# Kernel tuning notes

Hardware: AMD Instinct MI355X
Metric: run time of the kernel (lower is better)

## Reference

```python
import jax, jax.numpy as jnp
import numpy as np

N, F = 12288, 512
NEG_INF = jnp.float32(-1e9)  # matches Keras BaseDenseAttention mask additive constant


def setup_inputs() -> dict:
    key = jax.random.key(0)
    k1, k2 = jax.random.split(key)
    features = jax.random.normal(k1, (N, F), dtype=jnp.float32)
    A = jax.random.randint(k2, (N, N), 0, 2).astype(jnp.int32)
    return {"features": features, "A": A}


def reference(features, A):
    # Keras Attention with query=key=value=dropout(features); dropout is identity
    # at inference. use_scale=False -> plain dot-product scores, no 1/sqrt(d).
    scores = jnp.einsum("nf,mf->nm", features, features)          # [N, N]
    scores = jnp.where(A > 0, scores, NEG_INF)                    # mask non-edges
    attn = jax.nn.softmax(scores, axis=-1)                        # softmax over keys
    return jnp.einsum("nm,mf->nf", attn, features)                # [N, F]
```

## Files before the change

### kernel.cpp

```cpp
#include <hip/hip_runtime.h>
#include <cstddef>
#include <cstdint>

#define NN 12288
#define FF 512
#define NWORDS (NN / 32)
#define NKT (NN / 128)
#define CMP_BLOCKS ((NN * NWORDS) / 256)
#define PREP_BLOCKS ((NN / 32) * (FF / 32))

using half8 = __attribute__((ext_vector_type(8))) _Float16;
using half4 = __attribute__((ext_vector_type(4))) _Float16;
using f32x4 = __attribute__((ext_vector_type(4))) float;

constexpr float MASK_NEG = -1e9f;

__device__ __forceinline__ void gll16(const void* g, void* l) {
    __builtin_amdgcn_global_load_lds((const __attribute__((address_space(1))) void*)g,
                                     (__attribute__((address_space(3))) void*)l, 16, 0, 0);
}

#define PHASE(N)                                                        \
    do {                                                                \
        asm volatile("s_waitcnt vmcnt(" #N ")" ::: "memory");           \
        __builtin_amdgcn_s_barrier();                                   \
        __builtin_amdgcn_sched_barrier(0);                              \
    } while (0)

__global__ __launch_bounds__(256)
void prepass_fused(const int* __restrict__ Amat, uint32_t* __restrict__ Abits,
                   const float* __restrict__ in, _Float16* __restrict__ feath,
                   _Float16* __restrict__ featT) {
    const int bid = blockIdx.x;
    if (bid < CMP_BLOCKS) {
        const size_t W = (size_t)bid * 256 + threadIdx.x;
        const int4* p = reinterpret_cast<const int4*>(Amat + W * 32);
        uint32_t b = 0;
#pragma unroll
        for (int q = 0; q < 8; ++q) {
            const int4 v = p[q];
            b |= (uint32_t)(v.x > 0) << (4 * q + 0);
            b |= (uint32_t)(v.y > 0) << (4 * q + 1);
            b |= (uint32_t)(v.z > 0) << (4 * q + 2);
            b |= (uint32_t)(v.w > 0) << (4 * q + 3);
        }
        Abits[W] = b;
    } else {
        __shared__ float tile[32][33];
        const int b2 = bid - CMP_BLOCKS;
        const int bi = b2 % (NN / 32);
        const int bj = b2 / (NN / 32);
        const int r  = threadIdx.x >> 3;
        const int c4 = (threadIdx.x & 7) << 2;
        float4 v = *reinterpret_cast<const float4*>(in + (size_t)(bi * 32 + r) * FF + bj * 32 + c4);
        tile[r][c4 + 0] = v.x; tile[r][c4 + 1] = v.y; tile[r][c4 + 2] = v.z; tile[r][c4 + 3] = v.w;
        half4 hr;
        hr[0] = (_Float16)v.x; hr[1] = (_Float16)v.y; hr[2] = (_Float16)v.z; hr[3] = (_Float16)v.w;
        *reinterpret_cast<half4*>(feath + (size_t)(bi * 32 + r) * FF + bj * 32 + c4) = hr;
        __syncthreads();
        half4 h;
#pragma unroll
        for (int k = 0; k < 4; ++k) h[k] = (_Float16)tile[c4 + k][r];
        *reinterpret_cast<half4*>(featT + (size_t)(bj * 32 + r) * NN + bi * 32 + c4) = h;
    }
}

__global__ void cvt_feat_kernel(const float* __restrict__ in, _Float16* __restrict__ out) {
    const size_t i = ((size_t)blockIdx.x * blockDim.x + threadIdx.x) * 8;
    float4 x = *reinterpret_cast<const float4*>(in + i);
    float4 y = *reinterpret_cast<const float4*>(in + i + 4);
    half8 h;
    h[0] = (_Float16)x.x; h[1] = (_Float16)x.y; h[2] = (_Float16)x.z; h[3] = (_Float16)x.w;
    h[4] = (_Float16)y.x; h[5] = (_Float16)y.y; h[6] = (_Float16)y.z; h[7] = (_Float16)y.w;
    *reinterpret_cast<half8*>(out + i) = h;
}

__global__ __launch_bounds__(256)
void gemm1_exp(const _Float16* __restrict__ feath, const uint32_t* __restrict__ Abits,
               _Float16* __restrict__ Pmat, float* __restrict__ m_t, _Float16* __restrict__ s_t) {
    __shared__ alignas(16) _Float16 As[3][128 * 32];
    __shared__ alignas(16) _Float16 Bs[3][128 * 32];
    __shared__ alignas(16) float rowmax2[128][2];
    __shared__ alignas(16) float rowsum2[128][2];

    const int tid = threadIdx.x, lane = tid & 63, wid = tid >> 6;
    const int g = lane >> 4, a = lane & 15;
    const int wr = wid >> 1, wc = wid & 1;
    const int row0 = blockIdx.x * 128, col0 = blockIdx.y * 128;

    f32x4 acc[4][4];
#pragma unroll
    for (int i = 0; i < 4; ++i)
#pragma unroll
        for (int j = 0; j < 4; ++j) acc[i][j] = f32x4{0.f, 0.f, 0.f, 0.f};

    const int lr  = lane >> 2;
    const int sl  = lane & 3;
    const int lsw = (sl ^ ((lr >> 1) & 3)) * 8;
    const int rk  = (a >> 1) & 3;

    auto stage = [&](int buf, int t) {
#pragma unroll
        for (int c = 0; c < 2; ++c) {
            const int ch = wid * 2 + c;
            gll16(feath + (size_t)(row0 + ch * 16 + lr) * FF + t * 32 + lsw, &As[buf][ch * 512]);
            gll16(feath + (size_t)(col0 + ch * 16 + lr) * FF + t * 32 + lsw, &Bs[buf][ch * 512]);
        }
    };

    stage(0, 0);
    stage(1, 1);
#pragma unroll
    for (int t = 0; t < 16; ++t) {
        if (t < 15) PHASE(4);
        else        PHASE(0);
        const int cb = t % 3;
        half8 af[4], bf[4];
#pragma unroll
        for (int rf = 0; rf < 4; ++rf)
            af[rf] = *reinterpret_cast<const half8*>(&As[cb][(64 * wr + 16 * rf + a) * 32 + ((g ^ rk) << 3)]);
#pragma unroll
        for (int cf = 0; cf < 4; ++cf)
            bf[cf] = *reinterpret_cast<const half8*>(&Bs[cb][(64 * wc + 16 * cf + a) * 32 + ((g ^ rk) << 3)]);
#pragma unroll
        for (int rf = 0; rf < 4; ++rf)
#pragma unroll
            for (int cf = 0; cf < 4; ++cf)
                acc[rf][cf] = __builtin_amdgcn_mfma_f32_16x16x32_f16(af[rf], bf[cf], acc[rf][cf], 0, 0, 0);
        if (t + 2 < 16) stage((t + 2) % 3, t + 2);
    }

    const int cw0 = (col0 + 64 * wc) >> 5;
    uint2 am[4][4];
#pragma unroll
    for (int rf = 0; rf < 4; ++rf)
#pragma unroll
        for (int r = 0; r < 4; ++r) {
            const int grow = row0 + 64 * wr + 16 * rf + 4 * g + r;
            am[rf][r] = *reinterpret_cast<const uint2*>(&Abits[(size_t)grow * NWORDS + cw0]);
        }
#pragma unroll
    for (int rf = 0; rf < 4; ++rf)
#pragma unroll
        for (int r = 0; r < 4; ++r)
#pragma unroll
            for (int cf = 0; cf < 4; ++cf) {
                const uint32_t w = (cf < 2) ? am[rf][r].x : am[rf][r].y;
                const uint32_t bit = (w >> (a + 16 * (cf & 1))) & 1u;
                acc[rf][cf][r] = bit ? acc[rf][cf][r] : MASK_NEG;
            }

#pragma unroll
    for (int rf = 0; rf < 4; ++rf)
#pragma unroll
        for (int r = 0; r < 4; ++r) {
            float v = fmaxf(fmaxf(acc[rf][0][r], acc[rf][1][r]), fmaxf(acc[rf][2][r], acc[rf][3][r]));
            v = fmaxf(v, __shfl_xor(v, 1, 16));
            v = fmaxf(v, __shfl_xor(v, 2, 16));
            v = fmaxf(v, __shfl_xor(v, 4, 16));
            v = fmaxf(v, __shfl_xor(v, 8, 16));
            if (a == 0) rowmax2[64 * wr + 16 * rf + 4 * g + r][wc] = v;
        }
    __syncthreads();

#pragma unroll
    for (int rf = 0; rf < 4; ++rf)
#pragma unroll
        for (int r = 0; r < 4; ++r) {
            const int lrow = 64 * wr + 16 * rf + 4 * g + r;
            const float mt = fmaxf(rowmax2[lrow][0], rowmax2[lrow][1]);
            const size_t rbase = (size_t)(row0 + lrow) * NN + col0 + 64 * wc + a;
            float ps = 0.f;
#pragma unroll
            for (int cf = 0; cf < 4; ++cf) {
                const float p = __expf(acc[rf][cf][r] - mt);
                ps += p;
                Pmat[rbase + 16 * cf] = (_Float16)p;
            }
            ps += __shfl_xor(ps, 1, 16);
            ps += __shfl_xor(ps, 2, 16);
            ps += __shfl_xor(ps, 4, 16);
            ps += __shfl_xor(ps, 8, 16);
            if (a == 0) rowsum2[lrow][wc] = ps;
        }
    __syncthreads();
    if (tid < 128) {
        m_t[(size_t)blockIdx.y * NN + row0 + tid] = fmaxf(rowmax2[tid][0], rowmax2[tid][1]);
        s_t[(size_t)blockIdx.y * NN + row0 + tid] = (_Float16)(rowsum2[tid][0] + rowsum2[tid][1]);
    }
}

__global__ __launch_bounds__(256)
void stats_kernel(const float* __restrict__ m_t, const _Float16* __restrict__ s_t,
                  _Float16* __restrict__ sc_t, float* __restrict__ l_row) {
    const int r = blockIdx.x * 256 + threadIdx.x;
    float m = -3.0e38f;
#pragma unroll 4
    for (int kt = 0; kt < NKT; ++kt) m = fmaxf(m, m_t[(size_t)kt * NN + r]);
    float l = 0.f;
#pragma unroll 4
    for (int kt = 0; kt < NKT; ++kt) {
        const float e = __expf(m_t[(size_t)kt * NN + r] - m);
        sc_t[(size_t)kt * NN + r] = (_Float16)e;
        l += e * (float)s_t[(size_t)kt * NN + r];
    }
    l_row[r] = l;
}

__global__ __launch_bounds__(256)
void gemm2_scale(const _Float16* __restrict__ Pmat, const _Float16* __restrict__ featT,
                 const _Float16* __restrict__ sc_t, const float* __restrict__ l_row,
                 float* __restrict__ out) {
    __shared__ alignas(16) _Float16 As[2][128 * 64];
    __shared__ alignas(16) _Float16 Bs[2][64 * 64];

    const int tid = threadIdx.x, lane = tid & 63, wid = tid >> 6;
    const int g = lane >> 4, a = lane & 15;
    const int wr = wid >> 1, wc = wid & 1;
    const int row0 = blockIdx.x * 128, col0 = blockIdx.y * 64;

    f32x4 acc[4][2];
#pragma unroll
    for (int i = 0; i < 4; ++i) { acc[i][0] = f32x4{0.f,0.f,0.f,0.f}; acc[i][1] = f32x4{0.f,0.f,0.f,0.f}; }

    const int l8  = lane >> 3;
    const int sc8 = lane & 7;
    const int xk  = a & 7;
    const size_t scbase = row0 + 64 * wr + a;

    auto stage = [&](int buf, int t) {
#pragma unroll
        for (int c = 0; c < 4; ++c) {
            const int seg = wid * 4 + c;
            const int row = seg * 8 + l8;
            gll16(Pmat + (size_t)(row0 + row) * NN + t * 64 + ((sc8 ^ l8) << 3),
                  &As[buf][seg * 512]);
        }
#pragma unroll
        for (int c = 0; c < 2; ++c) {
            const int seg = wid * 2 + c;
            const int row = seg * 8 + l8;
            gll16(featT + (size_t)(col0 + row) * NN + t * 64 + ((sc8 ^ l8) << 3),
                  &Bs[buf][seg * 512]);
        }
    };

    _Float16 pend[4], sc[4];
#pragma unroll
    for (int rf = 0; rf < 4; ++rf) pend[rf] = sc_t[scbase + 16 * rf];

    stage(0, 0);
    __syncthreads();
    int buf = 0;
    for (int t = 0; t < 192; ++t) {
        if ((t & 1) == 0) {
#pragma unroll
            for (int rf = 0; rf < 4; ++rf) sc[rf] = pend[rf];
            const int ktn = (t >> 1) + 1;
            if (ktn < NKT) {
#pragma unroll
                for (int rf = 0; rf < 4; ++rf)
                    pend[rf] = sc_t[(size_t)ktn * NN + scbase + 16 * rf];
            }
        }
        if (t + 1 < 192) stage(buf ^ 1, t + 1);
#pragma unroll
        for (int kk = 0; kk < 2; ++kk) {
            const int c8r = ((kk << 2) + g) ^ xk;
            half8 af[4], bf[2];
#pragma unroll
            for (int rf = 0; rf < 4; ++rf) {
                const int row = 64 * wr + 16 * rf + a;
                af[rf] = *reinterpret_cast<const half8*>(&As[buf][row * 64 + (c8r << 3)]);
                af[rf] = af[rf] * sc[rf];
            }
#pragma unroll
            for (int cf = 0; cf < 2; ++cf) {
                const int row = 32 * wc + 16 * cf + a;
                bf[cf] = *reinterpret_cast<const half8*>(&Bs[buf][row * 64 + (c8r << 3)]);
            }
#pragma unroll
            for (int rf = 0; rf < 4; ++rf)
#pragma unroll
                for (int cf = 0; cf < 2; ++cf)
                    acc[rf][cf] = __builtin_amdgcn_mfma_f32_16x16x32_f16(af[rf], bf[cf], acc[rf][cf], 0, 0, 0);
        }
        __syncthreads();
        buf ^= 1;
    }

#pragma unroll
    for (int rf = 0; rf < 4; ++rf)
#pragma unroll
        for (int r = 0; r < 4; ++r) {
            const int grow = row0 + 64 * wr + 16 * rf + 4 * g + r;
            const float il = 1.0f / l_row[grow];
#pragma unroll
            for (int cf = 0; cf < 2; ++cf) {
                const int gcol = col0 + 32 * wc + 16 * cf + a;
                out[(size_t)grow * FF + gcol] = acc[rf][cf][r] * il;
            }
        }
}

constexpr int BM_ = 64;
constexpr int BN_ = 64;
constexpr int KV_STRIDE = 520;

template<bool RH>
__global__ __launch_bounds__(512, 2)
void attn_flash(const float* __restrict__ featf, const _Float16* __restrict__ feath,
                const int* __restrict__ Amat, float* __restrict__ out) {
    __shared__ alignas(16) _Float16 kv[BN_ * KV_STRIDE];
    __shared__ alignas(16) _Float16 pbuf[BM_][72];
    __shared__ alignas(16) float pmax[BM_][2];
    __shared__ alignas(16) float psum[BM_][2];
    __shared__ alignas(16) float m_s[BM_];
    __shared__ alignas(16) float l_s[BM_];
    __shared__ alignas(16) float rscale[BM_];

    const int tid  = threadIdx.x;
    const int lane = tid & 63;
    const int wid  = tid >> 6;
    const int g    = lane >> 4;
    const int a    = lane & 15;
    const int rg   = wid >> 1;
    const int ch   = wid & 1;
    const int qrow0 = blockIdx.x * BM_;

    half8 qf[16];
    {
        const int qr = qrow0 + 16 * rg + a;
#pragma unroll
        for (int ks = 0; ks < 16; ++ks) {
            const int f0 = 32 * ks + 8 * g;
            if constexpr (RH) {
                qf[ks] = *reinterpret_cast<const half8*>(feath + (size_t)qr * FF + f0);
            } else {
                const float* sp = featf + (size_t)qr * FF + f0;
                float4 x = *reinterpret_cast<const float4*>(sp);
                float4 y = *reinterpret_cast<const float4*>(sp + 4);
                half8 h;
                h[0] = (_Float16)x.x; h[1] = (_Float16)x.y; h[2] = (_Float16)x.z; h[3] = (_Float16)x.w;
                h[4] = (_Float16)y.x; h[5] = (_Float16)y.y; h[6] = (_Float16)y.z; h[7] = (_Float16)y.w;
                qf[ks] = h;
            }
        }
    }

    f32x4 acc[4][4];
#pragma unroll
    for (int i = 0; i < 4; ++i)
#pragma unroll
        for (int j = 0; j < 4; ++j) acc[i][j] = f32x4{0.f, 0.f, 0.f, 0.f};

    if (tid < BM_) { m_s[tid] = -INFINITY; l_s[tid] = 0.f; }
    __syncthreads();

    for (int kt = 0; kt < NN / BN_; ++kt) {
        const int key0 = kt * BN_;
#pragma unroll
        for (int i = 0; i < 8; ++i) {
            const int flat8 = tid + i * 512;
            const int key   = flat8 >> 6;
            const int b     = flat8 & 63;
            const int slot  = (b + (key >> 3)) & 63;
            _Float16* dst = &kv[key * KV_STRIDE + slot * 8];
            if constexpr (RH) {
                *reinterpret_cast<half8*>(dst) =
                    *reinterpret_cast<const half8*>(feath + (size_t)(key0 + key) * FF + b * 8);
            } else {
                const float* sp = featf + (size_t)(key0 + key) * FF + b * 8;
                float4 x = *reinterpret_cast<const float4*>(sp);
                float4 y = *reinterpret_cast<const float4*>(sp + 4);
                half8 h;
                h[0] = (_Float16)x.x; h[1] = (_Float16)x.y; h[2] = (_Float16)x.z; h[3] = (_Float16)x.w;
                h[4] = (_Float16)y.x; h[5] = (_Float16)y.y; h[6] = (_Float16)y.z; h[7] = (_Float16)y.w;
                *reinterpret_cast<half8*>(dst) = h;
            }
        }

        int am[2][4];
#pragma unroll
        for (int fc = 0; fc < 2; ++fc)
#pragma unroll
            for (int r = 0; r < 4; ++r) {
                const int arow = qrow0 + 16 * rg + 4 * g + r;
                const int acol = key0 + 32 * ch + 16 * fc + a;
                am[fc][r] = Amat[(size_t)arow * NN + acol];
            }
        __syncthreads();

        f32x4 s0{0.f, 0.f, 0.f, 0.f}, s1{0.f, 0.f, 0.f, 0.f};
        const int bk0 = 32 * ch + a;
        const int bk1 = bk0 + 16;
        const int kb0 = bk0 >> 3;
        const int kb1 = bk1 >> 3;
        const _Float16* kr0 = &kv[bk0 * KV_STRIDE];
        const _Float16* kr1 = &kv[bk1 * KV_STRIDE];
#pragma unroll
        for (int ks = 0; ks < 16; ++ks) {
            const int b = 4 * ks + g;
            const half8 bf0 = *reinterpret_cast<const half8*>(kr0 + (((b + kb0) & 63) << 3));
            const half8 bf1 = *reinterpret_cast<const half8*>(kr1 + (((b + kb1) & 63) << 3));
            s0 = __builtin_amdgcn_mfma_f32_16x16x32_f16(qf[ks], bf0, s0, 0, 0, 0);
            s1 = __builtin_amdgcn_mfma_f32_16x16x32_f16(qf[ks], bf1, s1, 0, 0, 0);
        }

        float sv[2][4];
#pragma unroll
        for (int r = 0; r < 4; ++r) {
            sv[0][r] = (am[0][r] > 0) ? s0[r] : MASK_NEG;
            sv[1][r] = (am[1][r] > 0) ? s1[r] : MASK_NEG;
        }
#pragma unroll
        for (int r = 0; r < 4; ++r) {
            float v = fmaxf(sv[0][r], sv[1][r]);
            v = fmaxf(v, __shfl_xor(v, 1, 16));
            v = fmaxf(v, __shfl_xor(v, 2, 16));
            v = fmaxf(v, __shfl_xor(v, 4, 16));
            v = fmaxf(v, __shfl_xor(v, 8, 16));
            if (a == 0) pmax[16 * rg + 4 * g + r][ch] = v;
        }
        __syncthreads();

#pragma unroll
        for (int r = 0; r < 4; ++r) {
            const int row = 16 * rg + 4 * g + r;
            const float mo = m_s[row];
            const float mn = fmaxf(mo, fmaxf(pmax[row][0], pmax[row][1]));
            const float p0 = __expf(sv[0][r] - mn);
            const float p1 = __expf(sv[1][r] - mn);
            pbuf[row][32 * ch + a]      = (_Float16)p0;
            pbuf[row][32 * ch + 16 + a] = (_Float16)p1;
            float ssum = p0 + p1;
            ssum += __shfl_xor(ssum, 1, 16);
            ssum += __shfl_xor(ssum, 2, 16);
            ssum += __shfl_xor(ssum, 4, 16);
            ssum += __shfl_xor(ssum, 8, 16);
            if (a == 0) psum[row][ch] = ssum;
        }
        __syncthreads();

        if (tid < BM_) {
            const float mo = m_s[tid];
            const float mn = fmaxf(mo, fmaxf(pmax[tid][0], pmax[tid][1]));
            const float sc = __expf(mo - mn);
            l_s[tid] = l_s[tid] * sc + psum[tid][0] + psum[tid][1];
            m_s[tid] = mn;
            rscale[tid] = sc;
        }
        __syncthreads();

#pragma unroll
        for (int rf = 0; rf < 4; ++rf) {
            const float4 scv = *reinterpret_cast<const float4*>(&rscale[16 * rf + 4 * g]);
#pragma unroll
            for (int cf = 0; cf < 4; ++cf) {
                acc[rf][cf][0] *= scv.x; acc[rf][cf][1] *= scv.y;
                acc[rf][cf][2] *= scv.z; acc[rf][cf][3] *= scv.w;
            }
        }
#pragma unroll
        for (int kk = 0; kk < 2; ++kk) {
            half8 af[4];
#pragma unroll
            for (int rf = 0; rf < 4; ++rf)
                af[rf] = *reinterpret_cast<const half8*>(&pbuf[16 * rf + a][32 * kk + 8 * g]);
            const int keybase = 32 * kk + 8 * g;
#pragma unroll
            for (int cf = 0; cf < 4; ++cf) {
                const int col  = 64 * wid + 16 * cf + a;
                const int slot = (((col >> 3) + 4 * kk + g) & 63);
                const _Float16* vb = &kv[(size_t)keybase * KV_STRIDE + (slot << 3) + (col & 7)];
                half8 bf;
#pragma unroll
                for (int j = 0; j < 8; ++j)
                    bf[j] = vb[j * KV_STRIDE];
#pragma unroll
                for (int rf = 0; rf < 4; ++rf)
                    acc[rf][cf] = __builtin_amdgcn_mfma_f32_16x16x32_f16(af[rf], bf, acc[rf][cf], 0, 0, 0);
            }
        }
        __syncthreads();
    }

#pragma unroll
    for (int rf = 0; rf < 4; ++rf) {
        const float4 lv = *reinterpret_cast<const float4*>(&l_s[16 * rf + 4 * g]);
        const float inv[4] = {1.f / lv.x, 1.f / lv.y, 1.f / lv.z, 1.f / lv.w};
#pragma unroll
        for (int cf = 0; cf < 4; ++cf) {
            const int col = 64 * wid + 16 * cf + a;
#pragma unroll
            for (int r = 0; r < 4; ++r) {
                out[(size_t)(qrow0 + 16 * rf + 4 * g + r) * FF + col] = acc[rf][cf][r] * inv[r];
            }
        }
    }
}

extern "C" void kernel_launch(void* const* d_in, const int* in_sizes, int n_in,
                              void* d_out, int out_size, void* d_ws, size_t ws_size,
                              hipStream_t stream) {
    const float* features = (const float*)d_in[0];
    const int*   Amat     = (const int*)d_in[1];
    float*       out      = (float*)d_out;

    const size_t P_bytes   = (size_t)NN * NN * 2;
    const size_t f16_bytes = (size_t)NN * FF * 2;
    const size_t sct_bytes = (size_t)NKT * NN * 2;
    const size_t st_bytes  = (size_t)NKT * NN * 2;
    const size_t l_bytes   = (size_t)NN * 4;
    const size_t total     = P_bytes + 2 * f16_bytes + sct_bytes + st_bytes + l_bytes;

    if (ws_size >= total) {
        char* w = (char*)d_ws;
        _Float16* Pmat  = (_Float16*)w;   w += P_bytes;
        _Float16* feath = (_Float16*)w;   w += f16_bytes;
        _Float16* featT = (_Float16*)w;   w += f16_bytes;
        _Float16* sc_t  = (_Float16*)w;   w += sct_bytes;
        _Float16* s_t   = (_Float16*)w;   w += st_bytes;
        float*    l_row = (float*)w;

        uint32_t* Abits = (uint32_t*)d_out;
        float*    m_t   = (float*)((char*)d_out + (size_t)NN * NWORDS * 4);

        prepass_fused<<<CMP_BLOCKS + PREP_BLOCKS, 256, 0, stream>>>(Amat, Abits, features, feath, featT);
        gemm1_exp<<<dim3(NN / 128, NN / 128), 256, 0, stream>>>(feath, Abits, Pmat, m_t, s_t);
        stats_kernel<<<NN / 256, 256, 0, stream>>>(m_t, s_t, sc_t, l_row);
        gemm2_scale<<<dim3(NN / 128, FF / 64), 256, 0, stream>>>(Pmat, featT, sc_t, l_row, out);
    } else if (ws_size >= f16_bytes) {
        _Float16* feath = (_Float16*)d_ws;
        cvt_feat_kernel<<<(NN * FF) / (256 * 8), 256, 0, stream>>>(features, feath);
        attn_flash<true><<<NN / BM_, 512, 0, stream>>>(features, feath, Amat, out);
    } else {
        attn_flash<false><<<NN / BM_, 512, 0, stream>>>(features, nullptr, Amat, out);
    }
}
```

Before: 742.3 us.

## Switch gemm1 to double-buffered BK=64 staging with XOR-swizzled LDS layout

```diff
diff --git a/kernel.cpp b/kernel.cpp
--- a/kernel.cpp
+++ b/kernel.cpp
@@ -19,13 +19,6 @@
     __builtin_amdgcn_global_load_lds((const __attribute__((address_space(1))) void*)g,
                                      (__attribute__((address_space(3))) void*)l, 16, 0, 0);
 }
-
-#define PHASE(N)                                                        \
-    do {                                                                \
-        asm volatile("s_waitcnt vmcnt(" #N ")" ::: "memory");           \
-        __builtin_amdgcn_s_barrier();                                   \
-        __builtin_amdgcn_sched_barrier(0);                              \
-    } while (0)
 
 __global__ __launch_bounds__(256)
 void prepass_fused(const int* __restrict__ Amat, uint32_t* __restrict__ Abits,
@@ -78,8 +71,8 @@
 __global__ __launch_bounds__(256)
 void gemm1_exp(const _Float16* __restrict__ feath, const uint32_t* __restrict__ Abits,
                _Float16* __restrict__ Pmat, float* __restrict__ m_t, _Float16* __restrict__ s_t) {
-    __shared__ alignas(16) _Float16 As[3][128 * 32];
-    __shared__ alignas(16) _Float16 Bs[3][128 * 32];
+    __shared__ alignas(16) _Float16 As[2][128 * 64];
+    __shared__ alignas(16) _Float16 Bs[2][128 * 64];
     __shared__ alignas(16) float rowmax2[128][2];
     __shared__ alignas(16) float rowsum2[128][2];
 
@@ -94,40 +87,50 @@
 #pragma unroll
         for (int j = 0; j < 4; ++j) acc[i][j] = f32x4{0.f, 0.f, 0.f, 0.f};
 
-    const int lr  = lane >> 2;
-    const int sl  = lane & 3;
-    const int lsw = (sl ^ ((lr >> 1) & 3)) * 8;
-    const int rk  = (a >> 1) & 3;
+    const int l8  = lane >> 3;
+    const int sc8 = lane & 7;
+    const int xk  = a & 7;
 
     auto stage = [&](int buf, int t) {
 #pragma unroll
-        for (int c = 0; c < 2; ++c) {
-            const int ch = wid * 2 + c;
-            gll16(feath + (size_t)(row0 + ch * 16 + lr) * FF + t * 32 + lsw, &As[buf][ch * 512]);
-            gll16(feath + (size_t)(col0 + ch * 16 + lr) * FF + t * 32 + lsw, &Bs[buf][ch * 512]);
+        for (int c = 0; c < 4; ++c) {
+            const int seg = wid * 4 + c;
+            const int row = seg * 8 + l8;
+            gll16(feath + (size_t)(row0 + row) * FF + t * 64 + ((sc8 ^ l8) << 3),
+                  &As[buf][seg * 512]);
+            gll16(feath + (size_t)(col0 + row) * FF + t * 64 + ((sc8 ^ l8) << 3),
+                  &Bs[buf][seg * 512]);
         }
     };
 
     stage(0, 0);
-    stage(1, 1);
-#pragma unroll
-    for (int t = 0; t < 16; ++t) {
-        if (t < 15) PHASE(4);
-        else        PHASE(0);
-        const int cb = t % 3;
-        half8 af[4], bf[4];
-#pragma unroll
-        for (int rf = 0; rf < 4; ++rf)
-            af[rf] = *reinterpret_cast<const half8*>(&As[cb][(64 * wr + 16 * rf + a) * 32 + ((g ^ rk) << 3)]);
-#pragma unroll
-        for (int cf = 0; cf < 4; ++cf)
-            bf[cf] = *reinterpret_cast<const half8*>(&Bs[cb][(64 * wc + 16 * cf + a) * 32 + ((g ^ rk) << 3)]);
-#pragma unroll
-        for (int rf = 0; rf < 4; ++rf)
-#pragma unroll
-            for (int cf = 0; cf < 4; ++cf)
-                acc[rf][cf] = __builtin_amdgcn_mfma_f32_16x16x32_f16(af[rf], bf[cf], acc[rf][cf], 0, 0, 0);
-        if (t + 2 < 16) stage((t + 2) % 3, t + 2);
+    __syncthreads();
+    int buf = 0;
+#pragma unroll
+    for (int t = 0; t < 8; ++t) {
+        if (t + 1 < 8) stage(buf ^ 1, t + 1);
+#pragma unroll
+        for (int kk = 0; kk < 2; ++kk) {
+            const int c8r = ((kk << 2) + g) ^ xk;
+            half8 af[4], bf[4];
+#pragma unroll
+            for (int rf = 0; rf < 4; ++rf) {
+                const int row = 64 * wr + 16 * rf + a;
+                af[rf] = *reinterpret_cast<const half8*>(&As[buf][row * 64 + (c8r << 3)]);
+            }
+#pragma unroll
+            for (int cf = 0; cf < 4; ++cf) {
+                const int row = 64 * wc + 16 * cf + a;
+                bf[cf] = *reinterpret_cast<const half8*>(&Bs[buf][row * 64 + (c8r << 3)]);
+            }
+#pragma unroll
+            for (int rf = 0; rf < 4; ++rf)
+#pragma unroll
+                for (int cf = 0; cf < 4; ++cf)
+                    acc[rf][cf] = __builtin_amdgcn_mfma_f32_16x16x32_f16(af[rf], bf[cf], acc[rf][cf], 0, 0, 0);
+        }
+        __syncthreads();
+        buf ^= 1;
     }
 
     const int cw0 = (col0 + 64 * wc) >> 5;
```

Result: no change. 729.4 us (-1.7%).
